# Kernel optimization log

Hardware: AMD Instinct MI355X
Metric: run time of the kernel (lower is better)

The kernel has to match this reference:

```python
import jax, jax.numpy as jnp
import numpy as np

B, S, D, H = 4, 1024, 1024, 16
HD = D // H  # 64
NEG = -10000000.0


def setup_inputs() -> dict:
    key = jax.random.key(0)
    ks = jax.random.split(key, 8)
    x = jax.random.normal(ks[0], (B, S, D), dtype=jnp.float32)
    adj = jax.random.randint(ks[1], (B, S, S), 0, 2).astype(jnp.float32)
    scale = 1.0 / np.sqrt(D)
    Wq = jax.random.normal(ks[2], (D, D), dtype=jnp.float32) * scale
    bq = jnp.zeros((D,), dtype=jnp.float32)
    Wk = jax.random.normal(ks[3], (D, D), dtype=jnp.float32) * scale
    bk = jnp.zeros((D,), dtype=jnp.float32)
    Wv = jax.random.normal(ks[4], (D, D), dtype=jnp.float32) * scale
    bv = jnp.zeros((D,), dtype=jnp.float32)
    return {"x": x, "adj": adj, "Wq": Wq, "bq": bq, "Wk": Wk, "bk": bk, "Wv": Wv, "bv": bv}


def reference(x, adj, Wq, bq, Wk, bk, Wv, bv):
    # QKV projections, split into heads: [B,S,D] -> [B,H,S,HD]
    def heads(t):
        return t.reshape(B, S, H, HD).transpose(0, 2, 1, 3)

    q = heads(x @ Wq + bq)
    k = heads(x @ Wk + bk)
    v = heads(x @ Wv + bv)

    # scaled scores [B,H,S,S]
    scores = jnp.einsum('bhqd,bhkd->bhqk', q, k) / jnp.sqrt(jnp.asarray(HD, x.dtype))
    # adjacency mask: 0 where adj>=0.5 else -1e7, broadcast over heads
    mask_add = jnp.where(adj < 0.5, jnp.asarray(NEG, x.dtype), jnp.asarray(0.0, x.dtype))
    scores = scores + mask_add[:, None, :, :]

    probs = jax.nn.softmax(scores, axis=-1)
    ctx = jnp.einsum('bhqk,bhkd->bhqd', probs, v)  # [B,H,S,HD]
    ctx = ctx.transpose(0, 2, 1, 3).reshape(B, S, D)
    h = jax.nn.relu(ctx)
    return (h, adj)
```

## Files before the change

### kernel.cpp

```cpp
#include <hip/hip_runtime.h>

constexpr int Bn  = 4;
constexpr int Sn  = 1024;
constexpr int Dn  = 1024;
constexpr int Hn  = 16;
constexpr int HDn = 64;

using short8   = __attribute__((ext_vector_type(8))) short;
using float4v  = __attribute__((ext_vector_type(4))) float;
using float16v = __attribute__((ext_vector_type(16))) float;

__device__ __forceinline__ ushort f2bf(float f) {
    union { float f; unsigned u; } v; v.f = f;
    unsigned r = v.u + 0x7fff + ((v.u >> 16) & 1);
    return (ushort)(r >> 16);
}

__device__ __forceinline__ void gload16(const void* g, void* l) {
    __builtin_amdgcn_global_load_lds(
        (const __attribute__((address_space(1))) void*)g,
        (__attribute__((address_space(3))) void*)l, 16, 0, 0);
}

__global__ __launch_bounds__(256) void prep(
    const float* __restrict__ x,
    const float* __restrict__ Wq, const float* __restrict__ Wk,
    const float* __restrict__ Wv, const float* __restrict__ adj,
    ushort* __restrict__ xb, ushort* __restrict__ Wt, uint* __restrict__ Mb,
    float* __restrict__ out)
{
    const int bx  = blockIdx.x;
    const int tid = threadIdx.x;
    __shared__ __align__(16) ushort pool[64 * 72];

    if (bx < 2048) {
        const size_t i = ((size_t)bx * 256 + tid) * 8;
        float4 a = *(const float4*)&x[i];
        float4 b = *(const float4*)&x[i + 4];
        ushort o[8] = {f2bf(a.x), f2bf(a.y), f2bf(a.z), f2bf(a.w),
                       f2bf(b.x), f2bf(b.y), f2bf(b.z), f2bf(b.w)};
        *(uint4*)&xb[i] = *(const uint4*)o;
    } else if (bx < 2816) {
        const int idx = bx - 2048;
        const int which = idx >> 8, rem = idx & 255;
        const float* __restrict__ W = (which == 0) ? Wq : (which == 1) ? Wk : Wv;
        ushort* __restrict__ O = Wt + (size_t)which * Dn * Dn;
        const int k0 = (rem & 15) * 64, n0 = (rem >> 4) * 64;
        ushort* T = pool;

        const int kl = tid >> 4, nl = (tid & 15) * 4;
#pragma unroll
        for (int p = 0; p < 4; ++p) {
            float4 w4 = *(const float4*)&W[(size_t)(k0 + p * 16 + kl) * Dn + n0 + nl];
            T[(nl + 0) * 72 + p * 16 + kl] = f2bf(w4.x);
            T[(nl + 1) * 72 + p * 16 + kl] = f2bf(w4.y);
            T[(nl + 2) * 72 + p * 16 + kl] = f2bf(w4.z);
            T[(nl + 3) * 72 + p * 16 + kl] = f2bf(w4.w);
        }
        __syncthreads();
        const int nr = tid >> 2, kc = (tid & 3) * 16;
        uint4 u0 = *(const uint4*)&T[nr * 72 + kc];
        uint4 u1 = *(const uint4*)&T[nr * 72 + kc + 8];
        *(uint4*)&O[(size_t)(n0 + nr) * Dn + k0 + kc]     = u0;
        *(uint4*)&O[(size_t)(n0 + nr) * Dn + k0 + kc + 8] = u1;
    } else {
        const int idx = bx - 2816;
        const int kt = idx & 15, qt = (idx >> 4) & 7, b = idx >> 7;
        char* msk = (char*)pool;

        float* ocopy = out + (size_t)Bn * Sn * Dn;
        const int r16 = tid >> 4, c4 = (tid & 15) * 4;
#pragma unroll
        for (int p = 0; p < 8; ++p) {
            const int row = p * 16 + r16;
            const size_t gi = ((size_t)b * Sn + qt * 128 + row) * Sn + kt * 64 + c4;
            float4 a = *(const float4*)&adj[gi];
            *(float4*)&ocopy[gi] = a;
            char* mr = &msk[row * 68 + c4];
            mr[0] = a.x >= 0.5f; mr[1] = a.y >= 0.5f;
            mr[2] = a.z >= 0.5f; mr[3] = a.w >= 0.5f;
        }
        __syncthreads();

        const int lane = tid & 63, w = tid >> 6;
        const int col = lane & 31, hi = lane >> 5;
        uint words[16];
#pragma unroll
        for (int mt = 0; mt < 2; ++mt)
#pragma unroll
            for (int pr = 0; pr < 8; ++pr) {
                const int r0 = 2 * pr;
                const int kl = mt * 32 + (r0 & 3) + 8 * (r0 >> 2) + 4 * hi;
                const char* mr = &msk[(w * 32 + col) * 68];
                words[mt * 8 + pr] = (mr[kl]     ? 0x0000FFFFu : 0u) |
                                     (mr[kl + 1] ? 0xFFFF0000u : 0u);
            }
        uint* dst = Mb + ((((size_t)(b * 8 + qt) * 16 + kt) * 4 + w) * 64 + lane) * 16;
#pragma unroll
        for (int c = 0; c < 4; ++c)
            *(uint4*)&dst[c * 4] =
                make_uint4(words[c*4], words[c*4+1], words[c*4+2], words[c*4+3]);
    }
}

__global__ __launch_bounds__(256) void qkv_gemm(
    const ushort* __restrict__ xb, const ushort* __restrict__ Wt,
    const float* __restrict__ bq, const float* __restrict__ bk,
    const float* __restrict__ bv,
    ushort* __restrict__ Qb, ushort* __restrict__ Kb, ushort* __restrict__ Vb)
{
    const int which = blockIdx.z;
    const ushort* __restrict__ Bw   = Wt + (size_t)which * Dn * Dn;
    const float* __restrict__  bias = (which == 0) ? bq : (which == 1) ? bk : bv;
    ushort* __restrict__       Out  = (which == 0) ? Qb : (which == 1) ? Kb : Vb;
    const float scale = (which == 0) ? 0.18033688011112042f : 1.0f;

    const int n0   = blockIdx.x * 128;
    const int m0   = blockIdx.y * 128;
    const int tid  = threadIdx.x;
    const int wave = tid >> 6;
    const int lane = tid & 63;
    const int wm   = wave >> 1;
    const int wn   = wave & 1;

    __shared__ __align__(16) ushort As[128 * 32];
    __shared__ __align__(16) ushort Bs[128 * 32];

    const int L0 = wave * 64 + lane;
    const int r0s = L0 >> 2, c0s = (L0 & 3) * 8;
    const int L1 = L0 + 256;
    const int r1s = L1 >> 2, c1s = (L1 & 3) * 8;

    const ushort* pA0 = &xb[(size_t)(m0 + r0s) * Dn + c0s];
    const ushort* pA1 = &xb[(size_t)(m0 + r1s) * Dn + c1s];
    const ushort* pB0 = &Bw[(size_t)(n0 + r0s) * Dn + c0s];
    const ushort* pB1 = &Bw[(size_t)(n0 + r1s) * Dn + c1s];

    char* ldsA0 = (char*)As + wave * 1024;
    char* ldsA1 = (char*)As + wave * 1024 + 4096;
    char* ldsB0 = (char*)Bs + wave * 1024;
    char* ldsB1 = (char*)Bs + wave * 1024 + 4096;

    const int mlane = lane & 15;
    const int kg    = (lane >> 4) * 8;

    float4v acc[4][4];
    const float4v z4 = {0.f, 0.f, 0.f, 0.f};
#pragma unroll
    for (int i = 0; i < 4; ++i)
#pragma unroll
        for (int j = 0; j < 4; ++j) acc[i][j] = z4;

    for (int k0 = 0; k0 < Dn; k0 += 32) {
        __syncthreads();
        gload16(pA0, ldsA0);
        gload16(pA1, ldsA1);
        gload16(pB0, ldsB0);
        gload16(pB1, ldsB1);
        pA0 += 32; pA1 += 32; pB0 += 32; pB1 += 32;
        __syncthreads();

        short8 af[4], bf[4];
#pragma unroll
        for (int i = 0; i < 4; ++i)
            af[i] = *(const short8*)&As[(wm * 64 + i * 16 + mlane) * 32 + kg];
#pragma unroll
        for (int j = 0; j < 4; ++j)
            bf[j] = *(const short8*)&Bs[(wn * 64 + j * 16 + mlane) * 32 + kg];
#pragma unroll
        for (int i = 0; i < 4; ++i)
#pragma unroll
            for (int j = 0; j < 4; ++j)
                acc[i][j] = __builtin_amdgcn_mfma_f32_16x16x32_bf16(af[i], bf[j], acc[i][j], 0, 0, 0);
    }

    const int rb  = (lane >> 4) * 4;
    const int col = lane & 15;
#pragma unroll
    for (int j = 0; j < 4; ++j) {
        const int n  = n0 + wn * 64 + j * 16 + col;
        const float bias_n = bias[n];
        const int h  = n >> 6;
        const int hd = n & 63;
#pragma unroll
        for (int i = 0; i < 4; ++i) {
#pragma unroll
            for (int r = 0; r < 4; ++r) {
                const int m = m0 + wm * 64 + i * 16 + rb + r;
                const int b = m >> 10;
                const int s = m & 1023;
                size_t addr;
                if (which == 2)
                    addr = (((size_t)(b * Hn + h)) * HDn + hd) * Sn + s;
                else
                    addr = (((size_t)(b * Hn + h)) * Sn + s) * HDn + hd;
                Out[addr] = f2bf((acc[i][j][r] + bias_n) * scale);
            }
        }
    }
}

__global__ __launch_bounds__(256, 2) void attn_mfma(
    const ushort* __restrict__ Q, const ushort* __restrict__ K,
    const ushort* __restrict__ Vt, const uint* __restrict__ Mw,
    float* __restrict__ out)
{
    const int qt = blockIdx.x, h = blockIdx.y, b = blockIdx.z;
    const int tid  = threadIdx.x;
    const int w    = tid >> 6, lane = tid & 63;
    const int col  = lane & 31, hi = lane >> 5;

    const size_t hb = ((size_t)(b * Hn + h)) * Sn * HDn;
    const ushort* Kg = K + hb;
    const ushort* Vg = Vt + hb;

    __shared__ __align__(16) ushort Ks[2][64 * 72];
    __shared__ __align__(16) ushort Vs[2][64 * 72];

    short8 qf[4];
#pragma unroll
    for (int kp = 0; kp < 4; ++kp)
        qf[kp] = *(const short8*)&Q[hb +
            (size_t)(qt * 128 + w * 32 + col) * HDn + kp * 16 + hi * 8];

    float16v o_[2];
#pragma unroll
    for (int dt = 0; dt < 2; ++dt)
#pragma unroll
        for (int r = 0; r < 16; ++r) o_[dt][r] = 0.f;
    float ls = 0.f;

    const int c0 = tid, c1 = tid + 256;
    const int la0 = (c0 >> 3) * 72 + (c0 & 7) * 8;
    const int la1 = (c1 >> 3) * 72 + (c1 & 7) * 8;

    uint4 k0 = *(const uint4*)&Kg[(size_t)(c0 >> 3) * HDn + (c0 & 7) * 8];
    uint4 k1 = *(const uint4*)&Kg[(size_t)(c1 >> 3) * HDn + (c1 & 7) * 8];
    uint4 v0 = *(const uint4*)&Vg[(size_t)(c0 >> 3) * Sn + (c0 & 7) * 8];
    uint4 v1 = *(const uint4*)&Vg[(size_t)(c1 >> 3) * Sn + (c1 & 7) * 8];
    *(uint4*)&Ks[0][la0] = k0;  *(uint4*)&Ks[0][la1] = k1;
    *(uint4*)&Vs[0][la0] = v0;  *(uint4*)&Vs[0][la1] = v1;
    __syncthreads();

    const uint* mbase = Mw + ((size_t)((b * 8 + qt) * 16) * 4 + w) * 1024 + lane * 16;

    for (int kt = 0; kt < 16; ++kt) {
        const int cur = kt & 1;
        if (kt < 15) {
            k0 = *(const uint4*)&Kg[(size_t)((kt + 1) * 64 + (c0 >> 3)) * HDn + (c0 & 7) * 8];
            k1 = *(const uint4*)&Kg[(size_t)((kt + 1) * 64 + (c1 >> 3)) * HDn + (c1 & 7) * 8];
            v0 = *(const uint4*)&Vg[(size_t)(c0 >> 3) * Sn + (kt + 1) * 64 + (c0 & 7) * 8];
            v1 = *(const uint4*)&Vg[(size_t)(c1 >> 3) * Sn + (kt + 1) * 64 + (c1 & 7) * 8];
        }
        const uint* mp = mbase + (size_t)kt * 4096;
        uint4 mk4[4];
        mk4[0] = *(const uint4*)(mp);
        mk4[1] = *(const uint4*)(mp + 4);
        mk4[2] = *(const uint4*)(mp + 8);
        mk4[3] = *(const uint4*)(mp + 12);
        const uint* mka = (const uint*)mk4;

#pragma unroll
        for (int mt = 0; mt < 2; ++mt) {
            float16v s_;
#pragma unroll
            for (int r = 0; r < 16; ++r) s_[r] = 0.f;
#pragma unroll
            for (int kp = 0; kp < 4; ++kp) {
                short8 ak = *(const short8*)&Ks[cur][(mt * 32 + col) * 72 + kp * 16 + hi * 8];
                s_ = __builtin_amdgcn_mfma_f32_32x32x16_bf16(ak, qf[kp], s_, 0, 0, 0);
            }

            unsigned up[8];
#pragma unroll
            for (int pr = 0; pr < 8; ++pr) {
                const unsigned e0 = __float_as_uint(exp2f(s_[2 * pr]))     + 0x8000u;
                const unsigned e1 = __float_as_uint(exp2f(s_[2 * pr + 1])) + 0x8000u;
                const unsigned u  = __builtin_amdgcn_perm(e1, e0, 0x07060302u) & mka[mt * 8 + pr];
                up[pr] = u;
                ls += __uint_as_float(u << 16) + __uint_as_float(u & 0xffff0000u);
            }

#pragma unroll
            for (int kh = 0; kh < 2; ++kh) {
                const unsigned a0 = up[kh * 4 + 0], a1 = up[kh * 4 + 1];
                const unsigned a2 = up[kh * 4 + 2], a3 = up[kh * 4 + 3];
                const unsigned t0 = (unsigned)__shfl_xor((int)(hi ? a0 : a2), 32, 64);
                const unsigned t1 = (unsigned)__shfl_xor((int)(hi ? a1 : a3), 32, 64);
                union { short8 s; unsigned u[4]; } f;
                f.u[0] = hi ? t0 : a0;
                f.u[1] = hi ? t1 : a1;
                f.u[2] = hi ? a2 : t0;
                f.u[3] = hi ? a3 : t1;
                const int kp = mt * 2 + kh;
#pragma unroll
                for (int dt = 0; dt < 2; ++dt) {
                    short8 av = *(const short8*)&Vs[cur][(dt * 32 + col) * 72 + kp * 16 + hi * 8];
                    o_[dt] = __builtin_amdgcn_mfma_f32_32x32x16_bf16(av, f.s, o_[dt], 0, 0, 0);
                }
            }
        }

        if (kt < 15) {
            const int nxt = cur ^ 1;
            *(uint4*)&Ks[nxt][la0] = k0;  *(uint4*)&Ks[nxt][la1] = k1;
            *(uint4*)&Vs[nxt][la0] = v0;  *(uint4*)&Vs[nxt][la1] = v1;
        }
        __syncthreads();
    }

    float l = ls + (float)__shfl_xor((float)ls, 32, 64);
    const float inv = 1.0f / l;
    const int q = qt * 128 + w * 32 + col;
    float* op = &out[((size_t)b * Sn + q) * Dn + h * 64];
#pragma unroll
    for (int dt = 0; dt < 2; ++dt)
#pragma unroll
        for (int rg = 0; rg < 4; ++rg) {
            const int d = dt * 32 + rg * 8 + hi * 4;
            float4 o4;
            o4.x = fmaxf(o_[dt][rg * 4 + 0] * inv, 0.0f);
            o4.y = fmaxf(o_[dt][rg * 4 + 1] * inv, 0.0f);
            o4.z = fmaxf(o_[dt][rg * 4 + 2] * inv, 0.0f);
            o4.w = fmaxf(o_[dt][rg * 4 + 3] * inv, 0.0f);
            *(float4*)&op[d] = o4;
        }
}

extern "C" void kernel_launch(void* const* d_in, const int* in_sizes, int n_in,
                              void* d_out, int out_size, void* d_ws, size_t ws_size,
                              hipStream_t stream)
{
    const float* x   = (const float*)d_in[0];
    const float* adj = (const float*)d_in[1];
    const float* Wq  = (const float*)d_in[2];
    const float* bq  = (const float*)d_in[3];
    const float* Wk  = (const float*)d_in[4];
    const float* bk  = (const float*)d_in[5];
    const float* Wv  = (const float*)d_in[6];
    const float* bv  = (const float*)d_in[7];
    float* out = (float*)d_out;

    ushort* xb = (ushort*)d_ws;
    ushort* Wt = xb + (size_t)Bn * Sn * Dn;
    ushort* Qb = Wt + (size_t)3 * Dn * Dn;
    ushort* Kb = Qb + (size_t)Bn * Hn * Sn * HDn;
    ushort* Vb = Kb + (size_t)Bn * Hn * Sn * HDn;
    uint*   Mb = (uint*)(Vb + (size_t)Bn * Hn * Sn * HDn);

    prep<<<dim3(3328), 256, 0, stream>>>(x, Wq, Wk, Wv, adj, xb, Wt, Mb, out);

    qkv_gemm<<<dim3(Dn / 128, (Bn * Sn) / 128, 3), 256, 0, stream>>>(
        xb, Wt, bq, bk, bv, Qb, Kb, Vb);

    attn_mfma<<<dim3(8, Hn, Bn), 256, 0, stream>>>(Qb, Kb, Vb, Mb, out);
}
```

Baseline: 188.2 us.

## Split key range across two wave groups per attention block and reduce via LDS

Attention blocks now have 512 threads in two 4-wave groups, each processing half of the key tiles with its own double-buffered K/V LDS. The partial outputs and row sums are combined through shared memory before the ReLU store. The grid is flattened with a swizzled block-to-(b,h,qt) mapping. This halves the serial key loop per wave, but the larger LDS footprint restricts blocks per CU.

```diff
diff --git a/kernel.cpp b/kernel.cpp
--- a/kernel.cpp
+++ b/kernel.cpp
@@ -200,28 +200,34 @@
     }
 }
 
-__global__ __launch_bounds__(256, 2) void attn_mfma(
+__global__ __launch_bounds__(512, 4) void attn_mfma(
     const ushort* __restrict__ Q, const ushort* __restrict__ K,
     const ushort* __restrict__ Vt, const uint* __restrict__ Mw,
     float* __restrict__ out)
 {
-    const int qt = blockIdx.x, h = blockIdx.y, b = blockIdx.z;
+    const int n  = blockIdx.x;
+    const int qt = (n >> 3) & 7;
+    const int bh = (n & 7) | ((n >> 6) << 3);
+    const int h  = bh & 15;
+    const int b  = bh >> 4;
+
     const int tid  = threadIdx.x;
     const int w    = tid >> 6, lane = tid & 63;
+    const int g    = w >> 2;
+    const int wq   = w & 3;
     const int col  = lane & 31, hi = lane >> 5;
 
     const size_t hb = ((size_t)(b * Hn + h)) * Sn * HDn;
     const ushort* Kg = K + hb;
     const ushort* Vg = Vt + hb;
 
-    __shared__ __align__(16) ushort Ks[2][64 * 72];
-    __shared__ __align__(16) ushort Vs[2][64 * 72];
+    __shared__ __align__(16) ushort KV[2][2][2][64 * 72];
 
     short8 qf[4];
 #pragma unroll
     for (int kp = 0; kp < 4; ++kp)
         qf[kp] = *(const short8*)&Q[hb +
-            (size_t)(qt * 128 + w * 32 + col) * HDn + kp * 16 + hi * 8];
+            (size_t)(qt * 128 + wq * 32 + col) * HDn + kp * 16 + hi * 8];
 
     float16v o_[2];
 #pragma unroll
@@ -230,29 +236,32 @@
         for (int r = 0; r < 16; ++r) o_[dt][r] = 0.f;
     float ls = 0.f;
 
-    const int c0 = tid, c1 = tid + 256;
+    const int t  = tid & 255;
+    const int c0 = t, c1 = t + 256;
     const int la0 = (c0 >> 3) * 72 + (c0 & 7) * 8;
     const int la1 = (c1 >> 3) * 72 + (c1 & 7) * 8;
-
-    uint4 k0 = *(const uint4*)&Kg[(size_t)(c0 >> 3) * HDn + (c0 & 7) * 8];
-    uint4 k1 = *(const uint4*)&Kg[(size_t)(c1 >> 3) * HDn + (c1 & 7) * 8];
-    uint4 v0 = *(const uint4*)&Vg[(size_t)(c0 >> 3) * Sn + (c0 & 7) * 8];
-    uint4 v1 = *(const uint4*)&Vg[(size_t)(c1 >> 3) * Sn + (c1 & 7) * 8];
-    *(uint4*)&Ks[0][la0] = k0;  *(uint4*)&Ks[0][la1] = k1;
-    *(uint4*)&Vs[0][la0] = v0;  *(uint4*)&Vs[0][la1] = v1;
+    const int kb  = g * 8;
+
+    uint4 k0 = *(const uint4*)&Kg[(size_t)(kb * 64 + (c0 >> 3)) * HDn + (c0 & 7) * 8];
+    uint4 k1 = *(const uint4*)&Kg[(size_t)(kb * 64 + (c1 >> 3)) * HDn + (c1 & 7) * 8];
+    uint4 v0 = *(const uint4*)&Vg[(size_t)(c0 >> 3) * Sn + kb * 64 + (c0 & 7) * 8];
+    uint4 v1 = *(const uint4*)&Vg[(size_t)(c1 >> 3) * Sn + kb * 64 + (c1 & 7) * 8];
+    *(uint4*)&KV[g][0][0][la0] = k0;  *(uint4*)&KV[g][0][0][la1] = k1;
+    *(uint4*)&KV[g][0][1][la0] = v0;  *(uint4*)&KV[g][0][1][la1] = v1;
     __syncthreads();
 
-    const uint* mbase = Mw + ((size_t)((b * 8 + qt) * 16) * 4 + w) * 1024 + lane * 16;
-
-    for (int kt = 0; kt < 16; ++kt) {
+    const uint* mbase = Mw + ((size_t)((b * 8 + qt) * 16) * 4 + wq) * 1024 + lane * 16;
+
+    for (int kt = 0; kt < 8; ++kt) {
         const int cur = kt & 1;
-        if (kt < 15) {
-            k0 = *(const uint4*)&Kg[(size_t)((kt + 1) * 64 + (c0 >> 3)) * HDn + (c0 & 7) * 8];
-            k1 = *(const uint4*)&Kg[(size_t)((kt + 1) * 64 + (c1 >> 3)) * HDn + (c1 & 7) * 8];
-            v0 = *(const uint4*)&Vg[(size_t)(c0 >> 3) * Sn + (kt + 1) * 64 + (c0 & 7) * 8];
-            v1 = *(const uint4*)&Vg[(size_t)(c1 >> 3) * Sn + (kt + 1) * 64 + (c1 & 7) * 8];
-        }
-        const uint* mp = mbase + (size_t)kt * 4096;
+        if (kt < 7) {
+            const int nk = (kb + kt + 1) * 64;
+            k0 = *(const uint4*)&Kg[(size_t)(nk + (c0 >> 3)) * HDn + (c0 & 7) * 8];
+            k1 = *(const uint4*)&Kg[(size_t)(nk + (c1 >> 3)) * HDn + (c1 & 7) * 8];
+            v0 = *(const uint4*)&Vg[(size_t)(c0 >> 3) * Sn + nk + (c0 & 7) * 8];
+            v1 = *(const uint4*)&Vg[(size_t)(c1 >> 3) * Sn + nk + (c1 & 7) * 8];
+        }
+        const uint* mp = mbase + (size_t)(kb + kt) * 4096;
         uint4 mk4[4];
         mk4[0] = *(const uint4*)(mp);
         mk4[1] = *(const uint4*)(mp + 4);
@@ -267,7 +276,7 @@
             for (int r = 0; r < 16; ++r) s_[r] = 0.f;
 #pragma unroll
             for (int kp = 0; kp < 4; ++kp) {
-                short8 ak = *(const short8*)&Ks[cur][(mt * 32 + col) * 72 + kp * 16 + hi * 8];
+                short8 ak = *(const short8*)&KV[g][cur][0][(mt * 32 + col) * 72 + kp * 16 + hi * 8];
                 s_ = __builtin_amdgcn_mfma_f32_32x32x16_bf16(ak, qf[kp], s_, 0, 0, 0);
             }
 
@@ -295,36 +304,56 @@
                 const int kp = mt * 2 + kh;
 #pragma unroll
                 for (int dt = 0; dt < 2; ++dt) {
-                    short8 av = *(const short8*)&Vs[cur][(dt * 32 + col) * 72 + kp * 16 + hi * 8];
+                    short8 av = *(const short8*)&KV[g][cur][1][(dt * 32 + col) * 72 + kp * 16 + hi * 8];
                     o_[dt] = __builtin_amdgcn_mfma_f32_32x32x16_bf16(av, f.s, o_[dt], 0, 0, 0);
                 }
             }
         }
 
-        if (kt < 15) {
+        if (kt < 7) {
             const int nxt = cur ^ 1;
-            *(uint4*)&Ks[nxt][la0] = k0;  *(uint4*)&Ks[nxt][la1] = k1;
-            *(uint4*)&Vs[nxt][la0] = v0;  *(uint4*)&Vs[nxt][la1] = v1;
-        }
-        __syncthreads();
-    }
-
-    float l = ls + (float)__shfl_xor((float)ls, 32, 64);
-    const float inv = 1.0f / l;
-    const int q = qt * 128 + w * 32 + col;
-    float* op = &out[((size_t)b * Sn + q) * Dn + h * 64];
-#pragma unroll
-    for (int dt = 0; dt < 2; ++dt)
-#pragma unroll
-        for (int rg = 0; rg < 4; ++rg) {
-            const int d = dt * 32 + rg * 8 + hi * 4;
-            float4 o4;
-            o4.x = fmaxf(o_[dt][rg * 4 + 0] * inv, 0.0f);
-            o4.y = fmaxf(o_[dt][rg * 4 + 1] * inv, 0.0f);
-            o4.z = fmaxf(o_[dt][rg * 4 + 2] * inv, 0.0f);
-            o4.w = fmaxf(o_[dt][rg * 4 + 3] * inv, 0.0f);
-            *(float4*)&op[d] = o4;
-        }
+            *(uint4*)&KV[g][nxt][0][la0] = k0;  *(uint4*)&KV[g][nxt][0][la1] = k1;
+            *(uint4*)&KV[g][nxt][1][la0] = v0;  *(uint4*)&KV[g][nxt][1][la1] = v1;
+        }
+        __syncthreads();
+    }
+
+    float* xo  = (float*)&KV[0][0][0][0];
+    float* lsx = xo + 4 * 64 * 36;
+    if (g == 1) {
+        float* dst = &xo[(wq * 64 + lane) * 36];
+#pragma unroll
+        for (int dt = 0; dt < 2; ++dt)
+#pragma unroll
+            for (int r4 = 0; r4 < 4; ++r4) {
+                float4 o4 = make_float4(o_[dt][r4 * 4 + 0], o_[dt][r4 * 4 + 1],
+                                        o_[dt][r4 * 4 + 2], o_[dt][r4 * 4 + 3]);
+                *(float4*)&dst[dt * 16 + r4 * 4] = o4;
+            }
+        lsx[wq * 64 + lane] = ls;
+    }
+    __syncthreads();
+    if (g == 0) {
+        const float* src = &xo[(wq * 64 + lane) * 36];
+        const float lt = ls + lsx[wq * 64 + lane];
+        const float l  = lt + (float)__shfl_xor(lt, 32, 64);
+        const float inv = 1.0f / l;
+        const int q = qt * 128 + wq * 32 + col;
+        float* op = &out[((size_t)b * Sn + q) * Dn + h * 64];
+#pragma unroll
+        for (int dt = 0; dt < 2; ++dt)
+#pragma unroll
+            for (int rg = 0; rg < 4; ++rg) {
+                float4 s4 = *(const float4*)&src[dt * 16 + rg * 4];
+                const int d = dt * 32 + rg * 8 + hi * 4;
+                float4 o4;
+                o4.x = fmaxf((o_[dt][rg * 4 + 0] + s4.x) * inv, 0.0f);
+                o4.y = fmaxf((o_[dt][rg * 4 + 1] + s4.y) * inv, 0.0f);
+                o4.z = fmaxf((o_[dt][rg * 4 + 2] + s4.z) * inv, 0.0f);
+                o4.w = fmaxf((o_[dt][rg * 4 + 3] + s4.w) * inv, 0.0f);
+                *(float4*)&op[d] = o4;
+            }
+    }
 }
 
 extern "C" void kernel_launch(void* const* d_in, const int* in_sizes, int n_in,
@@ -353,5 +382,5 @@
     qkv_gemm<<<dim3(Dn / 128, (Bn * Sn) / 128, 3), 256, 0, stream>>>(
         xb, Wt, bq, bk, bv, Qb, Kb, Vb);
 
-    attn_mfma<<<dim3(8, Hn, Bn), 256, 0, stream>>>(Qb, Kb, Vb, Mb, out);
-}
+    attn_mfma<<<dim3(512), 512, 0, stream>>>(Qb, Kb, Vb, Mb, out);
+}
```

Result: no change. 185.5 us (-1.5%).
